# Performance work log

Measured on AMD Instinct MI355X. Metric: run time of the kernel, lower is better.

Reference implementation:

```python
import jax, jax.numpy as jnp
import numpy as np

B, LQ, LK, H = 4, 256, 512, 256

def setup_inputs() -> dict:
    key = jax.random.key(0)
    ks = jax.random.split(key, 9)
    return {
        "query": jax.random.normal(ks[0], (B, LQ, H), dtype=jnp.float32),
        "key": jax.random.normal(ks[1], (B, LK, H), dtype=jnp.float32),
        "value": jax.random.normal(ks[2], (B, LK, H), dtype=jnp.float32),
        "mask": jax.random.randint(ks[3], (B, LK), 0, 2, dtype=jnp.int32),
        "Wq": jax.random.normal(ks[4], (H, H), dtype=jnp.float32) / np.sqrt(H),
        "bq": jnp.zeros((H,), dtype=jnp.float32),
        "Wk": jax.random.normal(ks[5], (H, H), dtype=jnp.float32) / np.sqrt(H),
        "bk": jnp.zeros((H,), dtype=jnp.float32),
        "v": jax.random.normal(ks[6], (H,), dtype=jnp.float32) / np.sqrt(H),
        "bv": jnp.zeros((), dtype=jnp.float32),
    }

def reference(query, key, value, mask, Wq, bq, Wk, bk, v, bv):
    # Linear projections: y = x @ W^T + b (torch nn.Linear convention)
    q = query @ Wq.T + bq            # [B, Lq, H]
    k = key @ Wk.T + bk              # [B, Lk, H]
    # Broadcast add -> tanh -> project to scalar with v
    s = jnp.tanh(q[:, :, None, :] + k[:, None, :, :])   # [B, Lq, Lk, H]
    scores = jnp.einsum('bqkh,h->bqk', s, v) + bv        # [B, Lq, Lk]
    scores = jnp.where(mask[:, None, :] == 0, -jnp.inf, scores)
    attn_weights = jax.nn.softmax(scores, axis=-1)       # [B, Lq, Lk]
    attn_output = jnp.einsum('bqk,bkh->bqh', attn_weights, value)
    return (attn_output, attn_weights)
```

## Files before the change

### kernel.cpp

```cpp
#include <hip/hip_runtime.h>
#include <math.h>

#define NB  4
#define NLQ 256
#define NLK 512
#define NH  256

#define SCALE_2LOG2E 2.885390081777927f
#define LOG2E        1.4426950408889634f

__global__ __launch_bounds__(256) void setup_kernel(
    const float* __restrict__ Wq, const float* __restrict__ Wk,
    const int* __restrict__ mask,
    float* __restrict__ Wtq, float* __restrict__ Wtk,
    int* __restrict__ act, int* __restrict__ nact)
{
    const int blk = blockIdx.x;
    const int t   = threadIdx.x;

    if (blk < 32) {
        __shared__ float ts[64][65];
        const int m    = blk >> 4;
        const int tile = blk & 15;
        const int h0 = (tile >> 2) * 64;
        const int c0 = (tile & 3) * 64;
        const float* W  = m ? Wk  : Wq;
        float*       Wt = m ? Wtk : Wtq;
        const int lr = t >> 4, lc = t & 15;
        #pragma unroll
        for (int i = 0; i < 4; ++i) {
            const int r = lr + 16 * i;
            const float4 d = *(const float4*)(W + (size_t)(h0 + r) * NH + c0 + lc * 4);
            ts[r][lc * 4 + 0] = d.x;
            ts[r][lc * 4 + 1] = d.y;
            ts[r][lc * 4 + 2] = d.z;
            ts[r][lc * 4 + 3] = d.w;
        }
        __syncthreads();
        #pragma unroll
        for (int i = 0; i < 4; ++i) {
            const int c = lr + 16 * i;
            float4 d;
            d.x = ts[lc * 4 + 0][c];
            d.y = ts[lc * 4 + 1][c];
            d.z = ts[lc * 4 + 2][c];
            d.w = ts[lc * 4 + 3][c];
            *(float4*)(Wt + (size_t)(c0 + c) * NH + h0 + lc * 4) = d;
        }
    } else if (blk < 32 + NB) {
        const int b = blk - 32;
        __shared__ int wcnt[8], wpre[9];
        const int lane = t & 63, wave = t >> 6;
        const int k1 = t, k2 = t + 256;
        const int m1 = mask[b * NLK + k1];
        const int m2 = mask[b * NLK + k2];
        const unsigned long long below = (1ULL << lane) - 1ULL;
        const unsigned long long bal1 = __ballot(m1 != 0);
        const unsigned long long bal2 = __ballot(m2 != 0);
        const int r1 = __popcll(bal1 & below);
        const int r2 = __popcll(bal2 & below);
        if (lane == 0) { wcnt[wave] = __popcll(bal1); wcnt[4 + wave] = __popcll(bal2); }
        __syncthreads();
        if (t == 0) {
            int s = 0;
            #pragma unroll
            for (int w = 0; w < 8; ++w) { wpre[w] = s; s += wcnt[w]; }
            wpre[8] = s;
        }
        __syncthreads();
        const int na = wpre[8];
        if (m1) act[b * NLK + wpre[wave]     + r1] = k1;
        if (m2) act[b * NLK + wpre[4 + wave] + r2] = k2;
        if (k1 >= na) act[b * NLK + k1] = 0;
        if (k2 >= na) act[b * NLK + k2] = 0;
        if (t == 0) nact[b] = na;
    }
}

__global__ __launch_bounds__(256) void prep_kernel(
    const float* __restrict__ query, const float* __restrict__ key,
    const float* __restrict__ Wtq, const float* __restrict__ bq,
    const float* __restrict__ Wtk, const float* __restrict__ bk,
    const int* __restrict__ act, const int* __restrict__ nact,
    float* __restrict__ qp, float* __restrict__ kp_ct)
{
    const int blk  = blockIdx.x;
    const int t    = threadIdx.x;
    const int wave = t >> 6;
    const int lane = t & 63;

    __shared__ float  xs[4][NH];
    __shared__ float4 ps[4][4][64];
    __shared__ int    ridx[4];

    const float *Wt, *bias;
    int b = 0, j0 = 0, r0 = 0, na = 0;
    const bool isq = (blk < NB * NLQ / 4);

    if (isq) {
        r0 = blk * 4;
        ((float4*)&xs[0][0])[t] = ((const float4*)(query + (size_t)r0 * NH))[t];
        Wt = Wtq; bias = bq;
    } else {
        b  = (blk - 256) >> 7;
        j0 = ((blk - 256) & 127) * 4;
        na = nact[b];
        if (j0 >= na) return;
        if (t < 4) ridx[t] = act[b * NLK + ((j0 + t < na) ? (j0 + t) : j0)];
        __syncthreads();
        const int r = t >> 6, c4 = t & 63;
        ((float4*)xs[r])[c4] =
            ((const float4*)(key + ((size_t)b * NLK + ridx[r]) * NH))[c4];
        Wt = Wtk; bias = bk;
    }
    __syncthreads();

    float4 acc[4];
    #pragma unroll
    for (int r = 0; r < 4; ++r) acc[r] = (float4){0.f, 0.f, 0.f, 0.f};

    const int cbase = wave * 64;
    #pragma unroll 4
    for (int cc = 0; cc < 64; ++cc) {
        const int c = cbase + cc;
        const float4 w = *(const float4*)(Wt + (size_t)c * NH + lane * 4);
        #pragma unroll
        for (int r = 0; r < 4; ++r) {
            const float xv = xs[r][c];
            acc[r].x = fmaf(xv, w.x, acc[r].x);
            acc[r].y = fmaf(xv, w.y, acc[r].y);
            acc[r].z = fmaf(xv, w.z, acc[r].z);
            acc[r].w = fmaf(xv, w.w, acc[r].w);
        }
    }
    #pragma unroll
    for (int r = 0; r < 4; ++r) ps[wave][r][lane] = acc[r];
    __syncthreads();

    const int r = wave, l = lane;
    const float4 p0 = ps[0][r][l], p1 = ps[1][r][l];
    const float4 p2 = ps[2][r][l], p3 = ps[3][r][l];
    const float4 bb = *(const float4*)(bias + l * 4);
    float4 o;
    o.x = (p0.x + p1.x + p2.x + p3.x + bb.x) * SCALE_2LOG2E;
    o.y = (p0.y + p1.y + p2.y + p3.y + bb.y) * SCALE_2LOG2E;
    o.z = (p0.z + p1.z + p2.z + p3.z + bb.z) * SCALE_2LOG2E;
    o.w = (p0.w + p1.w + p2.w + p3.w + bb.w) * SCALE_2LOG2E;

    if (isq) {
        *(float4*)(qp + (size_t)(r0 + r) * NH + l * 4) = o;
    } else if (j0 + r < na) {
        const int j = j0 + r;
        kp_ct[((size_t)b * NH + l * 4 + 0) * NLK + j] = o.x;
        kp_ct[((size_t)b * NH + l * 4 + 1) * NLK + j] = o.y;
        kp_ct[((size_t)b * NH + l * 4 + 2) * NLK + j] = o.z;
        kp_ct[((size_t)b * NH + l * 4 + 3) * NLK + j] = o.w;
    }
}

__global__ __launch_bounds__(256) void attn_kernel(
    const float* __restrict__ qp, const float* __restrict__ kp_ct,
    const float* __restrict__ value, const int* __restrict__ mask,
    const int* __restrict__ act, const int* __restrict__ nact,
    const float* __restrict__ vvec,
    float* __restrict__ out_o, float* __restrict__ out_w)
{
    __shared__ float sc0[NLK], sc1[NLK];
    __shared__ int   actl[NLK];
    __shared__ float pA[256], pB[256], pC[256], pD[256];

    const int blk  = blockIdx.x;
    const int b    = blk >> 7;
    const int q0   = (blk & 127) * 2;
    const int t    = threadIdx.x;
    const int lane = t & 63;
    const int wave = t >> 6;

    const int na = nact[b];
    actl[t]       = (t < na)       ? act[b * NLK + t]       : 0;
    actl[t + 256] = (t + 256 < na) ? act[b * NLK + t + 256] : 0;

    float* w0row = out_w + (size_t)(b * NLQ + q0) * NLK;
    float* w1row = w0row + NLK;
    if (!mask[b * NLK + t])       { w0row[t] = 0.f;       w1row[t] = 0.f; }
    if (!mask[b * NLK + t + 256]) { w0row[t + 256] = 0.f; w1row[t + 256] = 0.f; }

    const int hh    = t >> 7;
    const int p     = t & 127;
    const int hbase = hh * 128;
    const float* qr0 = qp + (size_t)(b * NLQ + q0) * NH + hbase;
    const float* qr1 = qr0 + NH;
    const float* vvh = vvec + hbase;
    const float* kb  = kp_ct + ((size_t)b * NH + hbase) * NLK;

    float a00 = 0.f, a01 = 0.f, a10 = 0.f, a11 = 0.f;
    #pragma unroll 4
    for (int c = 0; c < 128; ++c) {
        const float2 kx = *(const float2*)(kb + (size_t)c * NLK + 2 * p);
        const float qa = qr0[c], qb = qr1[c], vh = vvh[c];
        const float e0 = __builtin_amdgcn_exp2f(qa + kx.x);
        const float e1 = __builtin_amdgcn_exp2f(qa + kx.y);
        const float e2 = __builtin_amdgcn_exp2f(qb + kx.x);
        const float e3 = __builtin_amdgcn_exp2f(qb + kx.y);
        a00 = fmaf(vh, __builtin_amdgcn_rcpf(e0 + 1.f), a00);
        a01 = fmaf(vh, __builtin_amdgcn_rcpf(e1 + 1.f), a01);
        a10 = fmaf(vh, __builtin_amdgcn_rcpf(e2 + 1.f), a10);
        a11 = fmaf(vh, __builtin_amdgcn_rcpf(e3 + 1.f), a11);
    }
    pA[t] = a00; pB[t] = a01; pC[t] = a10; pD[t] = a11;
    __syncthreads();
    if (t < 128) {
        const int s = 2 * t;
        sc0[s]     = (s     < na) ? -2.f * (pA[t] + pA[t + 128]) : -INFINITY;
        sc0[s + 1] = (s + 1 < na) ? -2.f * (pB[t] + pB[t + 128]) : -INFINITY;
    } else {
        const int p2 = t - 128;
        const int s  = 2 * p2;
        sc1[s]     = (s     < na) ? -2.f * (pC[p2] + pC[p2 + 128]) : -INFINITY;
        sc1[s + 1] = (s + 1 < na) ? -2.f * (pD[p2] + pD[p2 + 128]) : -INFINITY;
    }

    if (na > 256) {
        __syncthreads();
        a00 = a01 = a10 = a11 = 0.f;
        const int s0 = 256 + 2 * p;
        if (s0 < na) {
            #pragma unroll 4
            for (int c = 0; c < 128; ++c) {
                const float2 kx = *(const float2*)(kb + (size_t)c * NLK + s0);
                const float qa = qr0[c], qb = qr1[c], vh = vvh[c];
                const float e0 = __builtin_amdgcn_exp2f(qa + kx.x);
                const float e1 = __builtin_amdgcn_exp2f(qa + kx.y);
                const float e2 = __builtin_amdgcn_exp2f(qb + kx.x);
                const float e3 = __builtin_amdgcn_exp2f(qb + kx.y);
                a00 = fmaf(vh, __builtin_amdgcn_rcpf(e0 + 1.f), a00);
                a01 = fmaf(vh, __builtin_amdgcn_rcpf(e1 + 1.f), a01);
                a10 = fmaf(vh, __builtin_amdgcn_rcpf(e2 + 1.f), a10);
                a11 = fmaf(vh, __builtin_amdgcn_rcpf(e3 + 1.f), a11);
            }
        }
        pA[t] = a00; pB[t] = a01; pC[t] = a10; pD[t] = a11;
        __syncthreads();
        if (t < 128) {
            const int s = 256 + 2 * t;
            sc0[s]     = (s     < na) ? -2.f * (pA[t] + pA[t + 128]) : -INFINITY;
            sc0[s + 1] = (s + 1 < na) ? -2.f * (pB[t] + pB[t + 128]) : -INFINITY;
        } else {
            const int p2 = t - 128;
            const int s  = 256 + 2 * p2;
            sc1[s]     = (s     < na) ? -2.f * (pC[p2] + pC[p2 + 128]) : -INFINITY;
            sc1[s + 1] = (s + 1 < na) ? -2.f * (pD[p2] + pD[p2 + 128]) : -INFINITY;
        }
    } else {
        sc0[256 + t] = -INFINITY;
        sc1[256 + t] = -INFINITY;
    }
    __syncthreads();

    if (wave < 2) {
        float* row = wave ? sc1 : sc0;
        float vals[8];
        float m = -INFINITY;
        #pragma unroll
        for (int j8 = 0; j8 < 8; ++j8) {
            vals[j8] = row[lane + j8 * 64];
            m = fmaxf(m, vals[j8]);
        }
        #pragma unroll
        for (int s = 32; s >= 1; s >>= 1)
            m = fmaxf(m, __shfl_xor(m, s, 64));
        float sum = 0.0f;
        #pragma unroll
        for (int j8 = 0; j8 < 8; ++j8) {
            vals[j8] = __builtin_amdgcn_exp2f((vals[j8] - m) * LOG2E);
            sum += vals[j8];
        }
        #pragma unroll
        for (int s = 32; s >= 1; s >>= 1)
            sum += __shfl_xor(sum, s, 64);
        const float inv = __builtin_amdgcn_rcpf(sum);
        float* wout = out_w + (size_t)(b * NLQ + q0 + wave) * NLK;
        #pragma unroll
        for (int j8 = 0; j8 < 8; ++j8) {
            const int jj = lane + j8 * 64;
            const float w = vals[j8] * inv;
            row[jj] = w;
            if (jj < na) wout[actl[jj]] = w;
        }
    }
    __syncthreads();

    {
        const float* vb = value + (size_t)b * NLK * NH + t;
        float o0 = 0.f, o1 = 0.f;
        const int n4 = (na + 3) >> 2;
        for (int j4 = 0; j4 < n4; ++j4) {
            const float4 w0 = ((const float4*)sc0)[j4];
            const float4 w1 = ((const float4*)sc1)[j4];
            const int4   aj = ((const int4*)actl)[j4];
            const float v0 = vb[(size_t)aj.x * NH];
            const float v1 = vb[(size_t)aj.y * NH];
            const float v2 = vb[(size_t)aj.z * NH];
            const float v3 = vb[(size_t)aj.w * NH];
            o0 = fmaf(w0.x, v0, o0); o1 = fmaf(w1.x, v0, o1);
            o0 = fmaf(w0.y, v1, o0); o1 = fmaf(w1.y, v1, o1);
            o0 = fmaf(w0.z, v2, o0); o1 = fmaf(w1.z, v2, o1);
            o0 = fmaf(w0.w, v3, o0); o1 = fmaf(w1.w, v3, o1);
        }
        out_o[(size_t)(b * NLQ + q0)     * NH + t] = o0;
        out_o[(size_t)(b * NLQ + q0 + 1) * NH + t] = o1;
    }
}

extern "C" void kernel_launch(void* const* d_in, const int* in_sizes, int n_in,
                              void* d_out, int out_size, void* d_ws, size_t ws_size,
                              hipStream_t stream) {
    const float* query = (const float*)d_in[0];
    const float* key   = (const float*)d_in[1];
    const float* value = (const float*)d_in[2];
    const int*   mask  = (const int*)  d_in[3];
    const float* Wq    = (const float*)d_in[4];
    const float* bq    = (const float*)d_in[5];
    const float* Wk    = (const float*)d_in[6];
    const float* bk    = (const float*)d_in[7];
    const float* v     = (const float*)d_in[8];

    float* out_o = (float*)d_out;
    float* out_w = out_o + NB * NLQ * NH;

    float* qp    = (float*)d_ws;
    float* kp_ct = qp + NB * NLQ * NH;
    int*   act   = (int*)(kp_ct + NB * NH * NLK);
    int*   nact  = act + NB * NLK;

    const size_t base = (size_t)(NB * NLQ * NH) + (size_t)(NB * NH * NLK)
                      + NB * NLK + NB;
    float* wtq;
    if (ws_size >= (base + 2 * NH * NH) * sizeof(float)) {
        wtq = (float*)d_ws + base;
    } else {
        wtq = out_w + (size_t)NB * NLQ * NLK - 2 * NH * NH;
    }
    float* wtk = wtq + NH * NH;

    setup_kernel<<<36, 256, 0, stream>>>(Wq, Wk, mask, wtq, wtk, act, nact);
    prep_kernel<<<NB * NLQ / 4 + NB * NLK / 4, 256, 0, stream>>>(
        query, key, wtq, bq, wtk, bk, act, nact, qp, kp_ct);
    attn_kernel<<<NB * NLQ / 2, 256, 0, stream>>>(
        qp, kp_ct, value, mask, act, nact, v, out_o, out_w);
}
```

Baseline: 130.2 us.

## Use 512-thread attention blocks with one key per thread and split PV reduction

The attention kernel moves to 512 threads so each thread computes the full-H additive score for one key, replacing the two-pass, half-H split with its shared-memory partial reductions. The weighted value sum is split across two 256-thread halves over the key range and combined through shared memory. This aims to raise parallelism per block and remove the extra sync passes. The cost is more register pressure per block, and the active-index list is now loaded without zero padding past the active count, so padded slots may hold stale indices.

```diff
diff --git a/kernel.cpp b/kernel.cpp
--- a/kernel.cpp
+++ b/kernel.cpp
@@ -158,7 +158,7 @@
     }
 }
 
-__global__ __launch_bounds__(256) void attn_kernel(
+__global__ __launch_bounds__(512) void attn_kernel(
     const float* __restrict__ qp, const float* __restrict__ kp_ct,
     const float* __restrict__ value, const int* __restrict__ mask,
     const int* __restrict__ act, const int* __restrict__ nact,
@@ -167,7 +167,7 @@
 {
     __shared__ float sc0[NLK], sc1[NLK];
     __shared__ int   actl[NLK];
-    __shared__ float pA[256], pB[256], pC[256], pD[256];
+    __shared__ float ph0[512], ph1[512];
 
     const int blk  = blockIdx.x;
     const int b    = blk >> 7;
@@ -177,84 +177,28 @@
     const int wave = t >> 6;
 
     const int na = nact[b];
-    actl[t]       = (t < na)       ? act[b * NLK + t]       : 0;
-    actl[t + 256] = (t + 256 < na) ? act[b * NLK + t + 256] : 0;
+    actl[t] = act[b * NLK + t];
 
     float* w0row = out_w + (size_t)(b * NLQ + q0) * NLK;
     float* w1row = w0row + NLK;
-    if (!mask[b * NLK + t])       { w0row[t] = 0.f;       w1row[t] = 0.f; }
-    if (!mask[b * NLK + t + 256]) { w0row[t + 256] = 0.f; w1row[t + 256] = 0.f; }
-
-    const int hh    = t >> 7;
-    const int p     = t & 127;
-    const int hbase = hh * 128;
-    const float* qr0 = qp + (size_t)(b * NLQ + q0) * NH + hbase;
+    if (!mask[b * NLK + t]) { w0row[t] = 0.f; w1row[t] = 0.f; }
+
+    const float* qr0 = qp + (size_t)(b * NLQ + q0) * NH;
     const float* qr1 = qr0 + NH;
-    const float* vvh = vvec + hbase;
-    const float* kb  = kp_ct + ((size_t)b * NH + hbase) * NLK;
-
-    float a00 = 0.f, a01 = 0.f, a10 = 0.f, a11 = 0.f;
-    #pragma unroll 4
-    for (int c = 0; c < 128; ++c) {
-        const float2 kx = *(const float2*)(kb + (size_t)c * NLK + 2 * p);
-        const float qa = qr0[c], qb = qr1[c], vh = vvh[c];
-        const float e0 = __builtin_amdgcn_exp2f(qa + kx.x);
-        const float e1 = __builtin_amdgcn_exp2f(qa + kx.y);
-        const float e2 = __builtin_amdgcn_exp2f(qb + kx.x);
-        const float e3 = __builtin_amdgcn_exp2f(qb + kx.y);
-        a00 = fmaf(vh, __builtin_amdgcn_rcpf(e0 + 1.f), a00);
-        a01 = fmaf(vh, __builtin_amdgcn_rcpf(e1 + 1.f), a01);
-        a10 = fmaf(vh, __builtin_amdgcn_rcpf(e2 + 1.f), a10);
-        a11 = fmaf(vh, __builtin_amdgcn_rcpf(e3 + 1.f), a11);
-    }
-    pA[t] = a00; pB[t] = a01; pC[t] = a10; pD[t] = a11;
-    __syncthreads();
-    if (t < 128) {
-        const int s = 2 * t;
-        sc0[s]     = (s     < na) ? -2.f * (pA[t] + pA[t + 128]) : -INFINITY;
-        sc0[s + 1] = (s + 1 < na) ? -2.f * (pB[t] + pB[t + 128]) : -INFINITY;
-    } else {
-        const int p2 = t - 128;
-        const int s  = 2 * p2;
-        sc1[s]     = (s     < na) ? -2.f * (pC[p2] + pC[p2 + 128]) : -INFINITY;
-        sc1[s + 1] = (s + 1 < na) ? -2.f * (pD[p2] + pD[p2 + 128]) : -INFINITY;
-    }
-
-    if (na > 256) {
-        __syncthreads();
-        a00 = a01 = a10 = a11 = 0.f;
-        const int s0 = 256 + 2 * p;
-        if (s0 < na) {
-            #pragma unroll 4
-            for (int c = 0; c < 128; ++c) {
-                const float2 kx = *(const float2*)(kb + (size_t)c * NLK + s0);
-                const float qa = qr0[c], qb = qr1[c], vh = vvh[c];
-                const float e0 = __builtin_amdgcn_exp2f(qa + kx.x);
-                const float e1 = __builtin_amdgcn_exp2f(qa + kx.y);
-                const float e2 = __builtin_amdgcn_exp2f(qb + kx.x);
-                const float e3 = __builtin_amdgcn_exp2f(qb + kx.y);
-                a00 = fmaf(vh, __builtin_amdgcn_rcpf(e0 + 1.f), a00);
-                a01 = fmaf(vh, __builtin_amdgcn_rcpf(e1 + 1.f), a01);
-                a10 = fmaf(vh, __builtin_amdgcn_rcpf(e2 + 1.f), a10);
-                a11 = fmaf(vh, __builtin_amdgcn_rcpf(e3 + 1.f), a11);
-            }
-        }
-        pA[t] = a00; pB[t] = a01; pC[t] = a10; pD[t] = a11;
-        __syncthreads();
-        if (t < 128) {
-            const int s = 256 + 2 * t;
-            sc0[s]     = (s     < na) ? -2.f * (pA[t] + pA[t + 128]) : -INFINITY;
-            sc0[s + 1] = (s + 1 < na) ? -2.f * (pB[t] + pB[t + 128]) : -INFINITY;
-        } else {
-            const int p2 = t - 128;
-            const int s  = 256 + 2 * p2;
-            sc1[s]     = (s     < na) ? -2.f * (pC[p2] + pC[p2 + 128]) : -INFINITY;
-            sc1[s + 1] = (s + 1 < na) ? -2.f * (pD[p2] + pD[p2 + 128]) : -INFINITY;
-        }
-    } else {
-        sc0[256 + t] = -INFINITY;
-        sc1[256 + t] = -INFINITY;
-    }
+    const float* kb  = kp_ct + (size_t)b * NH * NLK + t;
+
+    float a0 = 0.f, a1 = 0.f;
+    #pragma unroll 8
+    for (int c = 0; c < NH; ++c) {
+        const float kx = kb[(size_t)c * NLK];
+        const float qa = qr0[c], qb = qr1[c], vh = vvec[c];
+        const float e0 = __builtin_amdgcn_exp2f(qa + kx);
+        const float e1 = __builtin_amdgcn_exp2f(qb + kx);
+        a0 = fmaf(vh, __builtin_amdgcn_rcpf(e0 + 1.f), a0);
+        a1 = fmaf(vh, __builtin_amdgcn_rcpf(e1 + 1.f), a1);
+    }
+    sc0[t] = (t < na) ? -2.f * a0 : -INFINITY;
+    sc1[t] = (t < na) ? -2.f * a1 : -INFINITY;
     __syncthreads();
 
     if (wave < 2) {
@@ -291,10 +235,14 @@
     __syncthreads();
 
     {
-        const float* vb = value + (size_t)b * NLK * NH + t;
+        const int h    = t & 255;
+        const int half = t >> 8;
+        const int n4   = (na + 3) >> 2;
+        const int lo   = half * 64;
+        const int hi   = (n4 < lo + 64) ? n4 : (lo + 64);
+        const float* vb = value + (size_t)b * NLK * NH + h;
         float o0 = 0.f, o1 = 0.f;
-        const int n4 = (na + 3) >> 2;
-        for (int j4 = 0; j4 < n4; ++j4) {
+        for (int j4 = lo; j4 < hi; ++j4) {
             const float4 w0 = ((const float4*)sc0)[j4];
             const float4 w1 = ((const float4*)sc1)[j4];
             const int4   aj = ((const int4*)actl)[j4];
@@ -307,8 +255,13 @@
             o0 = fmaf(w0.z, v2, o0); o1 = fmaf(w1.z, v2, o1);
             o0 = fmaf(w0.w, v3, o0); o1 = fmaf(w1.w, v3, o1);
         }
-        out_o[(size_t)(b * NLQ + q0)     * NH + t] = o0;
-        out_o[(size_t)(b * NLQ + q0 + 1) * NH + t] = o1;
+        ph0[t] = o0;
+        ph1[t] = o1;
+    }
+    __syncthreads();
+    if (t < 256) {
+        out_o[(size_t)(b * NLQ + q0)     * NH + t] = ph0[t] + ph0[t + 256];
+        out_o[(size_t)(b * NLQ + q0 + 1) * NH + t] = ph1[t] + ph1[t + 256];
     }
 }
 
@@ -346,6 +299,6 @@
     setup_kernel<<<36, 256, 0, stream>>>(Wq, Wk, mask, wtq, wtk, act, nact);
     prep_kernel<<<NB * NLQ / 4 + NB * NLK / 4, 256, 0, stream>>>(
         query, key, wtq, bq, wtk, bk, act, nact, qp, kp_ct);
-    attn_kernel<<<NB * NLQ / 2, 256, 0, stream>>>(
+    attn_kernel<<<NB * NLQ / 2, 512, 0, stream>>>(
         qp, kp_ct, value, mask, act, nact, v, out_o, out_w);
 }
```

New measurement: 142.1 us. +9.2%, slower.
